# Kernel tuning notes

Hardware: AMD Instinct MI355X
Metric: run time of the kernel (lower is better)

The kernel has to match this reference:

```python
import jax, jax.numpy as jnp
import numpy as np

NUM_USERS = 100000
NUM_ITEMS = 50000
DIM = 128
NUM_EDGES = 600000


def setup_inputs() -> dict:
    key = jax.random.key(0)
    k1, k2, k3, k4, k5, k6 = jax.random.split(key, 6)
    u_emb = jax.random.normal(k1, (NUM_USERS, DIM), dtype=jnp.float32)
    i_emb = jax.random.normal(k2, (NUM_ITEMS, DIM), dtype=jnp.float32)
    user_idx = jax.random.randint(k3, (NUM_EDGES,), 0, NUM_USERS, dtype=jnp.int32)
    item_idx = jax.random.randint(k4, (NUM_EDGES,), 0, NUM_ITEMS, dtype=jnp.int32)
    edge_index = jnp.stack([user_idx, item_idx], axis=0)
    # weights in [0.2, 1.0] per docstring (unused in eval-mode forward)
    weights = 0.2 + 0.8 * jax.random.uniform(k5, (NUM_EDGES,), dtype=jnp.float32)
    attn_w = jax.random.normal(k6, (2 * DIM,), dtype=jnp.float32) * (1.0 / np.sqrt(2 * DIM))
    return {"u_emb": u_emb, "i_emb": i_emb, "edge_index": edge_index,
            "weights": weights, "attn_w": attn_w}


def _scatter_softmax(scores, idx, num_nodes):
    # numerically stable segment softmax over edges grouped by idx
    smax = jax.ops.segment_max(scores, idx, num_segments=num_nodes)  # [N]
    exp_s = jnp.exp(scores - smax[idx])                              # [E]
    ssum = jax.ops.segment_sum(exp_s, idx, num_segments=num_nodes)   # [N]
    return exp_s / (ssum[idx] + 1e-10)


def reference(u_emb, i_emb, edge_index, weights, attn_w):
    num_users = u_emb.shape[0]
    num_items = i_emb.shape[0]
    dim = u_emb.shape[1]
    user_idx, item_idx = edge_index[0], edge_index[1]

    # attn_projector(cat([u, i])) == u @ w_u + i @ w_i (no bias)
    w_u, w_i = attn_w[:dim], attn_w[dim:]
    raw = u_emb[user_idx] @ w_u + i_emb[item_idx] @ w_i  # [E]
    raw = jnp.where(raw >= 0, raw, 0.2 * raw)            # LeakyReLU(0.2)

    u_attn = _scatter_softmax(raw, user_idx, num_users)  # [E]
    i_attn = _scatter_softmax(raw, item_idx, num_items)  # [E]

    new_u = u_emb.at[user_idx].add(i_emb[item_idx] * u_attn[:, None])
    new_i = i_emb.at[item_idx].add(u_emb[user_idx] * i_attn[:, None])
    return new_u, new_i
```

## Files before the change

kernel.cpp:

```cpp
#include <hip/hip_runtime.h>

#define DIM 128
#define SCAN_BLK 1024

__device__ __forceinline__ unsigned short bf16rn(float f) {
    unsigned u = __float_as_uint(f);
    u += 0x7fffu + ((u >> 16) & 1u);
    return (unsigned short)(u >> 16);
}

__global__ void k_prep(const float* __restrict__ u_emb, const float* __restrict__ i_emb,
                       const float* __restrict__ attn_w, float* __restrict__ sdot,
                       ushort2* __restrict__ bemb, int nu, int n, int do_bf16) {
    int gw = (blockIdx.x * blockDim.x + threadIdx.x) >> 6;
    int lane = threadIdx.x & 63;
    if (gw >= n) return;
    const bool isU = gw < nu;
    const float2* row = (const float2*)(isU ? u_emb + (size_t)gw * DIM
                                            : i_emb + (size_t)(gw - nu) * DIM);
    const float2* wv  = (const float2*)(isU ? attn_w : attn_w + DIM);
    float2 a = row[lane];
    float2 b = wv[lane];
    float v = a.x * b.x + a.y * b.y;
    #pragma unroll
    for (int off = 32; off; off >>= 1) v += __shfl_down(v, off);
    if (lane == 0) sdot[gw] = v;
    if (do_bf16) {
        ushort2 h;
        h.x = bf16rn(a.x);
        h.y = bf16rn(a.y);
        bemb[(size_t)gw * (DIM / 2) + lane] = h;
    }
}

__global__ void k_count(const int* __restrict__ uidx, const int* __restrict__ iidx,
                        unsigned* __restrict__ cnt, unsigned* __restrict__ ranks,
                        int nu, int ne) {
    int e = blockIdx.x * blockDim.x + threadIdx.x;
    if (e >= ne) return;
    unsigned r0 = atomicAdd(&cnt[uidx[e]], 1u);
    unsigned r1 = atomicAdd(&cnt[nu + iidx[e]], 1u);
    ranks[e] = (r0 << 16) | (r1 & 0xffffu);
}

__global__ void k_scan1(const unsigned* __restrict__ cnt, unsigned* __restrict__ incl,
                        unsigned* __restrict__ bsum, int n) {
    __shared__ unsigned part[SCAN_BLK];
    int t = threadIdx.x;
    int j = blockIdx.x * SCAN_BLK + t;
    unsigned v = (j < n) ? cnt[j] : 0u;
    part[t] = v;
    __syncthreads();
    for (int d = 1; d < SCAN_BLK; d <<= 1) {
        unsigned w = (t >= d) ? part[t - d] : 0u;
        __syncthreads();
        part[t] += w;
        __syncthreads();
    }
    if (j < n) incl[j] = part[t];
    if (t == SCAN_BLK - 1) bsum[blockIdx.x] = part[t];
}

__global__ void k_scan2(unsigned* __restrict__ bsum, int nb) {
    __shared__ unsigned part[SCAN_BLK];
    int t = threadIdx.x;
    unsigned v = (t < nb) ? bsum[t] : 0u;
    part[t] = v;
    __syncthreads();
    for (int d = 1; d < SCAN_BLK; d <<= 1) {
        unsigned w = (t >= d) ? part[t - d] : 0u;
        __syncthreads();
        part[t] += w;
        __syncthreads();
    }
    if (t < nb) bsum[t] = part[t] - v;
}

__global__ void k_scan3(const unsigned* __restrict__ cnt, const unsigned* __restrict__ incl,
                        const unsigned* __restrict__ bsum,
                        unsigned* __restrict__ off, int n) {
    int j = blockIdx.x * blockDim.x + threadIdx.x;
    if (j >= n) return;
    off[j] = incl[j] - cnt[j] + bsum[j / SCAN_BLK];
}

__global__ void k_fill(const int* __restrict__ uidx, const int* __restrict__ iidx,
                       const unsigned* __restrict__ off, const unsigned* __restrict__ ranks,
                       int* __restrict__ nbr, int nu, int ne) {
    int e = blockIdx.x * blockDim.x + threadIdx.x;
    if (e >= ne) return;
    int u = uidx[e], i = iidx[e];
    unsigned rk = ranks[e];
    nbr[off[u]      + (rk >> 16)]     = nu + i;
    nbr[off[nu + i] + (rk & 0xffffu)] = u;
}

__global__ void k_accum_bf16(const float* __restrict__ u_emb, const float* __restrict__ i_emb,
                             const uint4* __restrict__ bemb, const float* __restrict__ sdot,
                             const unsigned* __restrict__ off, const unsigned* __restrict__ cnt,
                             const int* __restrict__ nbr,
                             float* __restrict__ out, int nu, int n) {
    int gw = (blockIdx.x * blockDim.x + threadIdx.x) >> 6;
    int lane = threadIdx.x & 63;
    if (gw >= n) return;
    int q   = lane >> 4;
    int l16 = lane & 15;
    float sd_self = sdot[gw];
    unsigned s = off[gw];
    unsigned d = cnt[gw];
    float acc[8] = {0.f, 0.f, 0.f, 0.f, 0.f, 0.f, 0.f, 0.f};
    float wsum = 0.f;

    for (unsigned base = 0; base < d; base += 64) {
        unsigned chunk = d - base; if (chunk > 64) chunk = 64;
        int   o = 0;
        float w = 0.f;
        if (lane < (int)chunk) {
            o = nbr[s + base + lane];
            float r = sd_self + sdot[o];
            r = (r >= 0.f) ? r : 0.2f * r;
            w = expf(r);
        }
        unsigned j = 0;
        #pragma unroll 2
        for (; j + 4 <= chunk; j += 4) {
            int   src = (int)j + q;
            int   oj = __shfl(o, src);
            float wj = __shfl(w, src);
            uint4 h = bemb[(size_t)oj * (DIM / 8) + l16];
            wsum += wj;
            acc[0] += wj * __uint_as_float(h.x << 16);
            acc[1] += wj * __uint_as_float(h.x & 0xffff0000u);
            acc[2] += wj * __uint_as_float(h.y << 16);
            acc[3] += wj * __uint_as_float(h.y & 0xffff0000u);
            acc[4] += wj * __uint_as_float(h.z << 16);
            acc[5] += wj * __uint_as_float(h.z & 0xffff0000u);
            acc[6] += wj * __uint_as_float(h.w << 16);
            acc[7] += wj * __uint_as_float(h.w & 0xffff0000u);
        }
        unsigned rem = chunk - j;
        if (rem) {
            int   src = (int)(j + (unsigned)q);
            int   oj = __shfl(o, src);
            float wj = __shfl(w, src);
            if ((unsigned)q < rem) {
                uint4 h = bemb[(size_t)oj * (DIM / 8) + l16];
                wsum += wj;
                acc[0] += wj * __uint_as_float(h.x << 16);
                acc[1] += wj * __uint_as_float(h.x & 0xffff0000u);
                acc[2] += wj * __uint_as_float(h.y << 16);
                acc[3] += wj * __uint_as_float(h.y & 0xffff0000u);
                acc[4] += wj * __uint_as_float(h.z << 16);
                acc[5] += wj * __uint_as_float(h.z & 0xffff0000u);
                acc[6] += wj * __uint_as_float(h.w << 16);
                acc[7] += wj * __uint_as_float(h.w & 0xffff0000u);
            }
        }
    }

    #pragma unroll
    for (int m = 16; m <= 32; m <<= 1) {
        wsum += __shfl_xor(wsum, m);
        #pragma unroll
        for (int k = 0; k < 8; ++k) acc[k] += __shfl_xor(acc[k], m);
    }

    if (q == 0) {
        float inv = 1.f / (wsum + 1e-10f);
        const float* self = (gw < nu) ? u_emb + (size_t)gw * DIM
                                      : i_emb + (size_t)(gw - nu) * DIM;
        const float4* sr = (const float4*)self;
        float4 s0 = sr[2 * l16];
        float4 s1 = sr[2 * l16 + 1];
        s0.x += acc[0] * inv; s0.y += acc[1] * inv;
        s0.z += acc[2] * inv; s0.w += acc[3] * inv;
        s1.x += acc[4] * inv; s1.y += acc[5] * inv;
        s1.z += acc[6] * inv; s1.w += acc[7] * inv;
        float4* orow = (float4*)(out + (size_t)gw * DIM);
        orow[2 * l16]     = s0;
        orow[2 * l16 + 1] = s1;
    }
}

__global__ void k_accum_f32(const float* __restrict__ u_emb, const float* __restrict__ i_emb,
                            const float* __restrict__ sdot,
                            const unsigned* __restrict__ off, const unsigned* __restrict__ cnt,
                            const int* __restrict__ nbr,
                            float* __restrict__ out, int nu, int n) {
    int gw = (blockIdx.x * blockDim.x + threadIdx.x) >> 6;
    int lane = threadIdx.x & 63;
    if (gw >= n) return;
    float sd_self = sdot[gw];
    unsigned s = off[gw];
    unsigned d = cnt[gw];
    float2 acc = make_float2(0.f, 0.f);
    float wsum = 0.f;
    for (unsigned base = 0; base < d; base += 64) {
        unsigned chunk = d - base; if (chunk > 64) chunk = 64;
        int   o = 0;
        float w = 0.f;
        if (lane < (int)chunk) {
            o = nbr[s + base + lane];
            float r = sd_self + sdot[o];
            r = (r >= 0.f) ? r : 0.2f * r;
            w = expf(r);
        }
        for (unsigned j = 0; j < chunk; ++j) {
            int   oj = __shfl(o, (int)j);
            float wj = __shfl(w, (int)j);
            const float* base_ = (oj < nu) ? u_emb + (size_t)oj * DIM
                                           : i_emb + (size_t)(oj - nu) * DIM;
            float2 vj = ((const float2*)base_)[lane];
            wsum += wj;
            acc.x += wj * vj.x;
            acc.y += wj * vj.y;
        }
    }
    float inv = 1.f / (wsum + 1e-10f);
    const float* self = (gw < nu) ? u_emb + (size_t)gw * DIM
                                  : i_emb + (size_t)(gw - nu) * DIM;
    float2 sv = ((const float2*)self)[lane];
    sv.x += acc.x * inv;
    sv.y += acc.y * inv;
    ((float2*)(out + (size_t)gw * DIM))[lane] = sv;
}

extern "C" void kernel_launch(void* const* d_in, const int* in_sizes, int n_in,
                              void* d_out, int out_size, void* d_ws, size_t ws_size,
                              hipStream_t stream) {
    const float* u_emb  = (const float*)d_in[0];
    const float* i_emb  = (const float*)d_in[1];
    const int*   edge   = (const int*)d_in[2];
    const float* attn_w = (const float*)d_in[4];

    const int nu = in_sizes[0] / DIM;
    const int ni = in_sizes[1] / DIM;
    const int ne = in_sizes[3];
    const int n  = nu + ni;

    const int* uidx = edge;
    const int* iidx = edge + ne;

    float* out = (float*)d_out;

    char* ws = (char*)d_ws;
    size_t used = 0;
    auto take = [&](size_t bytes) {
        char* p = ws + used;
        used += (bytes + 15) & ~size_t(15);
        return p;
    };
    float*    sdot  = (float*)   take((size_t)n * sizeof(float));
    unsigned* cnt   = (unsigned*)take((size_t)n * sizeof(unsigned));
    unsigned* off   = (unsigned*)take((size_t)n * sizeof(unsigned));
    unsigned* incl  = (unsigned*)take((size_t)n * sizeof(unsigned));
    unsigned* bsum  = (unsigned*)take((size_t)SCAN_BLK * sizeof(unsigned));
    unsigned* ranks = (unsigned*)take((size_t)ne * sizeof(unsigned));
    int*      nbr   = (int*)     take((size_t)2 * ne * sizeof(int));
    size_t bembBytes = (size_t)n * DIM * 2;
    const int do_bf16 = (used + bembBytes <= ws_size) ? 1 : 0;
    void* bemb = do_bf16 ? (void*)take(bembBytes) : nullptr;

    const int nb = (n + SCAN_BLK - 1) / SCAN_BLK;

    hipMemsetAsync(cnt, 0, (size_t)n * sizeof(unsigned), stream);

    k_prep<<<(n + 3) / 4, 256, 0, stream>>>(u_emb, i_emb, attn_w, sdot,
                                            (ushort2*)bemb, nu, n, do_bf16);

    k_count<<<(ne + 255) / 256, 256, 0, stream>>>(uidx, iidx, cnt, ranks, nu, ne);

    k_scan1<<<nb, SCAN_BLK, 0, stream>>>(cnt, incl, bsum, n);
    k_scan2<<<1, SCAN_BLK, 0, stream>>>(bsum, nb);
    k_scan3<<<(n + 255) / 256, 256, 0, stream>>>(cnt, incl, bsum, off, n);

    k_fill<<<(ne + 255) / 256, 256, 0, stream>>>(uidx, iidx, off, ranks, nbr, nu, ne);

    if (do_bf16)
        k_accum_bf16<<<(n + 3) / 4, 256, 0, stream>>>(u_emb, i_emb, (const uint4*)bemb,
                                                      sdot, off, cnt, nbr, out, nu, n);
    else
        k_accum_f32<<<(n + 3) / 4, 256, 0, stream>>>(u_emb, i_emb, sdot, off, cnt,
                                                     nbr, out, nu, n);
}
```

Before: 187.2 us.

## Fuse prep and count kernels; persistent accum with next-node prefetch

Merges the score/bf16 prep kernel and the edge-count kernel into one launch that splits its blocks by role, removing a launch and letting the two phases overlap. The bf16 accumulation kernel becomes a grid-stride persistent kernel with 2048 blocks. Each wave prefetches the next node's offset, degree, neighbor ids and neighbor scores while it processes the current node, hiding the dependent-load latency. It also switches to fast __expf and a fmaxf-based LeakyReLU, which adds register pressure and slightly changes the rounding of the exponent.

```diff
diff --git a/kernel.cpp b/kernel.cpp
--- a/kernel.cpp
+++ b/kernel.cpp
@@ -9,10 +9,21 @@
     return (unsigned short)(u >> 16);
 }
 
-__global__ void k_prep(const float* __restrict__ u_emb, const float* __restrict__ i_emb,
-                       const float* __restrict__ attn_w, float* __restrict__ sdot,
-                       ushort2* __restrict__ bemb, int nu, int n, int do_bf16) {
-    int gw = (blockIdx.x * blockDim.x + threadIdx.x) >> 6;
+__global__ void k_prep_count(const float* __restrict__ u_emb, const float* __restrict__ i_emb,
+                             const float* __restrict__ attn_w, float* __restrict__ sdot,
+                             ushort2* __restrict__ bemb,
+                             const int* __restrict__ uidx, const int* __restrict__ iidx,
+                             unsigned* __restrict__ cnt, unsigned* __restrict__ ranks,
+                             int nu, int n, int ne, int nbCount, int do_bf16) {
+    if ((int)blockIdx.x < nbCount) {
+        int e = blockIdx.x * blockDim.x + threadIdx.x;
+        if (e >= ne) return;
+        unsigned r0 = atomicAdd(&cnt[uidx[e]], 1u);
+        unsigned r1 = atomicAdd(&cnt[nu + iidx[e]], 1u);
+        ranks[e] = (r0 << 16) | (r1 & 0xffffu);
+        return;
+    }
+    int gw = ((blockIdx.x - nbCount) * blockDim.x + threadIdx.x) >> 6;
     int lane = threadIdx.x & 63;
     if (gw >= n) return;
     const bool isU = gw < nu;
@@ -33,16 +44,6 @@
     }
 }
 
-__global__ void k_count(const int* __restrict__ uidx, const int* __restrict__ iidx,
-                        unsigned* __restrict__ cnt, unsigned* __restrict__ ranks,
-                        int nu, int ne) {
-    int e = blockIdx.x * blockDim.x + threadIdx.x;
-    if (e >= ne) return;
-    unsigned r0 = atomicAdd(&cnt[uidx[e]], 1u);
-    unsigned r1 = atomicAdd(&cnt[nu + iidx[e]], 1u);
-    ranks[e] = (r0 << 16) | (r1 & 0xffffu);
-}
-
 __global__ void k_scan1(const unsigned* __restrict__ cnt, unsigned* __restrict__ incl,
                         unsigned* __restrict__ bsum, int n) {
     __shared__ unsigned part[SCAN_BLK];
@@ -100,50 +101,38 @@
                              const unsigned* __restrict__ off, const unsigned* __restrict__ cnt,
                              const int* __restrict__ nbr,
                              float* __restrict__ out, int nu, int n) {
-    int gw = (blockIdx.x * blockDim.x + threadIdx.x) >> 6;
+    int gw   = (blockIdx.x * blockDim.x + threadIdx.x) >> 6;
     int lane = threadIdx.x & 63;
-    if (gw >= n) return;
-    int q   = lane >> 4;
-    int l16 = lane & 15;
-    float sd_self = sdot[gw];
-    unsigned s = off[gw];
-    unsigned d = cnt[gw];
-    float acc[8] = {0.f, 0.f, 0.f, 0.f, 0.f, 0.f, 0.f, 0.f};
-    float wsum = 0.f;
-
-    for (unsigned base = 0; base < d; base += 64) {
-        unsigned chunk = d - base; if (chunk > 64) chunk = 64;
-        int   o = 0;
-        float w = 0.f;
-        if (lane < (int)chunk) {
-            o = nbr[s + base + lane];
-            float r = sd_self + sdot[o];
-            r = (r >= 0.f) ? r : 0.2f * r;
-            w = expf(r);
-        }
-        unsigned j = 0;
-        #pragma unroll 2
-        for (; j + 4 <= chunk; j += 4) {
-            int   src = (int)j + q;
-            int   oj = __shfl(o, src);
-            float wj = __shfl(w, src);
-            uint4 h = bemb[(size_t)oj * (DIM / 8) + l16];
-            wsum += wj;
-            acc[0] += wj * __uint_as_float(h.x << 16);
-            acc[1] += wj * __uint_as_float(h.x & 0xffff0000u);
-            acc[2] += wj * __uint_as_float(h.y << 16);
-            acc[3] += wj * __uint_as_float(h.y & 0xffff0000u);
-            acc[4] += wj * __uint_as_float(h.z << 16);
-            acc[5] += wj * __uint_as_float(h.z & 0xffff0000u);
-            acc[6] += wj * __uint_as_float(h.w << 16);
-            acc[7] += wj * __uint_as_float(h.w & 0xffff0000u);
-        }
-        unsigned rem = chunk - j;
-        if (rem) {
-            int   src = (int)(j + (unsigned)q);
-            int   oj = __shfl(o, src);
-            float wj = __shfl(w, src);
-            if ((unsigned)q < rem) {
+    int nwav = (gridDim.x * blockDim.x) >> 6;
+    int q = lane >> 4, l16 = lane & 15;
+
+    int node = gw;
+    if (node >= n) return;
+
+    unsigned sC = off[node], dC = cnt[node];
+    float ssC = sdot[node];
+    int oC = 0; float sdC = 0.f;
+    {
+        unsigned dc = dC < 64u ? dC : 64u;
+        if ((unsigned)lane < dc) { oC = nbr[sC + lane]; sdC = sdot[oC]; }
+    }
+
+    while (true) {
+        int nnode = node + nwav;
+        unsigned sN = 0, dN = 0; float ssN = 0.f; int oN = 0; float sdN = 0.f;
+        if (nnode < n) {
+            sN = off[nnode]; dN = cnt[nnode]; ssN = sdot[nnode];
+            unsigned dn = dN < 64u ? dN : 64u;
+            if ((unsigned)lane < dn) { oN = nbr[sN + lane]; sdN = sdot[oN]; }
+        }
+
+        float acc[8] = {0.f, 0.f, 0.f, 0.f, 0.f, 0.f, 0.f, 0.f};
+        float wsum = 0.f;
+
+        auto doQuad = [&](int oArr, float wArr, int srcIdx, bool active) {
+            int   oj = __shfl(oArr, srcIdx);
+            float wj = __shfl(wArr, srcIdx);
+            if (active) {
                 uint4 h = bemb[(size_t)oj * (DIM / 8) + l16];
                 wsum += wj;
                 acc[0] += wj * __uint_as_float(h.x << 16);
@@ -155,30 +144,60 @@
                 acc[6] += wj * __uint_as_float(h.w << 16);
                 acc[7] += wj * __uint_as_float(h.w & 0xffff0000u);
             }
-        }
-    }
-
-    #pragma unroll
-    for (int m = 16; m <= 32; m <<= 1) {
-        wsum += __shfl_xor(wsum, m);
+        };
+
+        unsigned d0 = dC < 64u ? dC : 64u;
+        float w = 0.f;
+        if ((unsigned)lane < d0) {
+            float r = ssC + sdC;
+            r = fmaxf(r, 0.2f * r);
+            w = __expf(r);
+        }
+        unsigned j = 0;
+        #pragma unroll 4
+        for (; j + 4 <= d0; j += 4) doQuad(oC, w, (int)j + q, true);
+        if (j < d0)                 doQuad(oC, w, (int)(j + (unsigned)q), (unsigned)q < d0 - j);
+
+        for (unsigned base = 64; base < dC; base += 64) {
+            unsigned chunk = dC - base; if (chunk > 64) chunk = 64;
+            int o2 = 0; float w2 = 0.f;
+            if ((unsigned)lane < chunk) {
+                o2 = nbr[sC + base + lane];
+                float r = ssC + sdot[o2];
+                r = fmaxf(r, 0.2f * r);
+                w2 = __expf(r);
+            }
+            unsigned jj = 0;
+            for (; jj + 4 <= chunk; jj += 4) doQuad(o2, w2, (int)jj + q, true);
+            if (jj < chunk)                  doQuad(o2, w2, (int)(jj + (unsigned)q), (unsigned)q < chunk - jj);
+        }
+
         #pragma unroll
-        for (int k = 0; k < 8; ++k) acc[k] += __shfl_xor(acc[k], m);
-    }
-
-    if (q == 0) {
-        float inv = 1.f / (wsum + 1e-10f);
-        const float* self = (gw < nu) ? u_emb + (size_t)gw * DIM
-                                      : i_emb + (size_t)(gw - nu) * DIM;
-        const float4* sr = (const float4*)self;
-        float4 s0 = sr[2 * l16];
-        float4 s1 = sr[2 * l16 + 1];
-        s0.x += acc[0] * inv; s0.y += acc[1] * inv;
-        s0.z += acc[2] * inv; s0.w += acc[3] * inv;
-        s1.x += acc[4] * inv; s1.y += acc[5] * inv;
-        s1.z += acc[6] * inv; s1.w += acc[7] * inv;
-        float4* orow = (float4*)(out + (size_t)gw * DIM);
-        orow[2 * l16]     = s0;
-        orow[2 * l16 + 1] = s1;
+        for (int m = 16; m <= 32; m <<= 1) {
+            wsum += __shfl_xor(wsum, m);
+            #pragma unroll
+            for (int k = 0; k < 8; ++k) acc[k] += __shfl_xor(acc[k], m);
+        }
+
+        if (q == 0) {
+            float inv = 1.f / (wsum + 1e-10f);
+            const float* self = (node < nu) ? u_emb + (size_t)node * DIM
+                                            : i_emb + (size_t)(node - nu) * DIM;
+            const float4* sr = (const float4*)self;
+            float4 s0 = sr[2 * l16];
+            float4 s1 = sr[2 * l16 + 1];
+            s0.x += acc[0] * inv; s0.y += acc[1] * inv;
+            s0.z += acc[2] * inv; s0.w += acc[3] * inv;
+            s1.x += acc[4] * inv; s1.y += acc[5] * inv;
+            s1.z += acc[6] * inv; s1.w += acc[7] * inv;
+            float4* orow = (float4*)(out + (size_t)node * DIM);
+            orow[2 * l16]     = s0;
+            orow[2 * l16 + 1] = s1;
+        }
+
+        if (nnode >= n) break;
+        node = nnode;
+        sC = sN; dC = dN; ssC = ssN; oC = oN; sdC = sdN;
     }
 }
 
@@ -202,8 +221,8 @@
         if (lane < (int)chunk) {
             o = nbr[s + base + lane];
             float r = sd_self + sdot[o];
-            r = (r >= 0.f) ? r : 0.2f * r;
-            w = expf(r);
+            r = fmaxf(r, 0.2f * r);
+            w = __expf(r);
         }
         for (unsigned j = 0; j < chunk; ++j) {
             int   oj = __shfl(o, (int)j);
@@ -261,14 +280,16 @@
     const int do_bf16 = (used + bembBytes <= ws_size) ? 1 : 0;
     void* bemb = do_bf16 ? (void*)take(bembBytes) : nullptr;
 
-    const int nb = (n + SCAN_BLK - 1) / SCAN_BLK;
+    const int nb      = (n + SCAN_BLK - 1) / SCAN_BLK;
+    const int nbCount = (ne + 255) / 256;
+    const int nbPrep  = (n + 3) / 4;
 
     hipMemsetAsync(cnt, 0, (size_t)n * sizeof(unsigned), stream);
 
-    k_prep<<<(n + 3) / 4, 256, 0, stream>>>(u_emb, i_emb, attn_w, sdot,
-                                            (ushort2*)bemb, nu, n, do_bf16);
-
-    k_count<<<(ne + 255) / 256, 256, 0, stream>>>(uidx, iidx, cnt, ranks, nu, ne);
+    k_prep_count<<<nbCount + nbPrep, 256, 0, stream>>>(u_emb, i_emb, attn_w, sdot,
+                                                       (ushort2*)bemb, uidx, iidx,
+                                                       cnt, ranks, nu, n, ne,
+                                                       nbCount, do_bf16);
 
     k_scan1<<<nb, SCAN_BLK, 0, stream>>>(cnt, incl, bsum, n);
     k_scan2<<<1, SCAN_BLK, 0, stream>>>(bsum, nb);
@@ -277,8 +298,8 @@
     k_fill<<<(ne + 255) / 256, 256, 0, stream>>>(uidx, iidx, off, ranks, nbr, nu, ne);
 
     if (do_bf16)
-        k_accum_bf16<<<(n + 3) / 4, 256, 0, stream>>>(u_emb, i_emb, (const uint4*)bemb,
-                                                      sdot, off, cnt, nbr, out, nu, n);
+        k_accum_bf16<<<2048, 256, 0, stream>>>(u_emb, i_emb, (const uint4*)bemb,
+                                               sdot, off, cnt, nbr, out, nu, n);
     else
         k_accum_f32<<<(n + 3) / 4, 256, 0, stream>>>(u_emb, i_emb, sdot, off, cnt,
                                                      nbr, out, nu, n);
```

After: 175.5 us. 6.2% less time.
